# Performance work log

Hardware: AMD Instinct MI355X
Metric: run time of the kernel (lower is better)

Reference implementation:

```python
import jax, jax.numpy as jnp
import numpy as np

N_NODES = 100000

def gcn_conv(x, W, b, src, dst, n_nodes):
    # PyG GCNConv: out = D^{-1/2} (A + I) D^{-1/2} (x W) + b, deg includes self-loop
    h = x @ W  # [N, H]
    ones = jnp.ones(src.shape[0], dtype=x.dtype)
    deg = jax.ops.segment_sum(ones, dst, num_segments=n_nodes) + 1.0  # +1 self-loop
    dinv = jax.lax.rsqrt(deg)  # deg >= 1, no zeros
    norm = dinv[src] * dinv[dst]  # [E]
    msg = h[src] * norm[:, None]  # [E, H] gather + scale
    agg = jax.ops.segment_sum(msg, dst, num_segments=n_nodes)  # scatter-add
    self_contrib = h * (dinv * dinv)[:, None]  # self-loop term norm = dinv_i^2
    return agg + self_contrib + b


def setup_inputs() -> dict:
    key = jax.random.key(0)
    ks = jax.random.split(key, 6)
    F_IN, H, E = 128, 128, 1600000
    x = jax.random.normal(ks[0], (N_NODES, F_IN), dtype=jnp.float32)
    edge_index = jax.random.randint(ks[1], (2, E), 0, N_NODES, dtype=jnp.int32)
    s = 1.0 / np.sqrt(F_IN)
    W1 = jax.random.normal(ks[2], (F_IN, H), dtype=jnp.float32) * s
    b1 = jnp.zeros((H,), dtype=jnp.float32)
    W2 = jax.random.normal(ks[3], (H, H), dtype=jnp.float32) * (1.0 / np.sqrt(H))
    b2 = jnp.zeros((H,), dtype=jnp.float32)
    Wlin = jax.random.normal(ks[4], (H, 1), dtype=jnp.float32) * (1.0 / np.sqrt(H))
    blin = jnp.zeros((1,), dtype=jnp.float32)
    return {"x": x, "edge_index": edge_index, "W1": W1, "b1": b1,
            "W2": W2, "b2": b2, "Wlin": Wlin, "blin": blin}


def reference(x, edge_index, W1, b1, W2, b2, Wlin, blin):
    src, dst = edge_index[0], edge_index[1]
    h = gcn_conv(x, W1, b1, src, dst, N_NODES)
    h = jax.nn.relu(h)
    h = gcn_conv(h, W2, b2, src, dst, N_NODES)
    h = jax.nn.relu(h)
    out = h @ Wlin + blin  # [N, 1]
    return out.squeeze(-1)  # [N]
```

## Files before the change

### kernel.cpp

```cpp
#include <hip/hip_runtime.h>
#include <hip/hip_fp16.h>

#define NFEAT 128

typedef _Float16 v8hf __attribute__((ext_vector_type(8)));
typedef _Float16 v4hf __attribute__((ext_vector_type(4)));
typedef float v4f __attribute__((ext_vector_type(4)));

__global__ void k_deg_rank_w(const int* __restrict__ dst, int* __restrict__ deg,
                             int* __restrict__ rank, int E, int N,
                             const float* __restrict__ W1, const float* __restrict__ W2,
                             _Float16* __restrict__ Wt1, _Float16* __restrict__ Wt2) {
  int e = blockIdx.x * blockDim.x + threadIdx.x;
  if (e < E) rank[e] = atomicAdd(&deg[dst[e]], 1);
  else if (e < E + N) rank[e] = atomicAdd(&deg[e - E], 1);
  else if (e < E + N + 32768) {
    int idx = e - E - N;
    const float* W = (idx < 16384) ? W1 : W2;
    _Float16* Wt = (idx < 16384) ? Wt1 : Wt2;
    int i = idx & 16383;
    int k = i >> 7, n = i & 127;
    Wt[n * 128 + k] = (_Float16)W[k * 128 + n];
  }
}

__device__ __forceinline__ int wave_incl_scan(int v, int lane) {
  #pragma unroll
  for (int off = 1; off < 64; off <<= 1) {
    int t = __shfl_up(v, off, 64);
    if (lane >= off) v += t;
  }
  return v;
}

__global__ __launch_bounds__(256) void k_scan_blocks(const int* __restrict__ deg,
    int* __restrict__ base, int* __restrict__ partials, int n) {
  __shared__ int lds[4];
  const int tid = threadIdx.x;
  const int lane = tid & 63;
  const int wv = tid >> 6;
  int i0 = (blockIdx.x << 9) + (tid << 1);
  int a = (i0 < n) ? deg[i0] : 0;
  int b = (i0 + 1 < n) ? deg[i0 + 1] : 0;
  int inc = wave_incl_scan(a + b, lane);
  if (lane == 63) lds[wv] = inc;
  __syncthreads();
  int woff = 0, tot = 0;
  #pragma unroll
  for (int w = 0; w < 4; w++) {
    int t = lds[w];
    tot += t;
    if (w < wv) woff += t;
  }
  int ex = woff + inc - (a + b);
  const int N1 = n + 1;
  if (i0 < N1) base[i0] = ex;
  if (i0 + 1 < N1) base[i0 + 1] = ex + a;
  if (tid == 255) partials[blockIdx.x] = tot;
}

__global__ __launch_bounds__(256) void k_scan_partials(int* __restrict__ partials,
                                                       int nb) {
  __shared__ int lds[4];
  const int tid = threadIdx.x;
  const int lane = tid & 63;
  const int wv = tid >> 6;
  int v = (tid < nb) ? partials[tid] : 0;
  int inc = wave_incl_scan(v, lane);
  if (lane == 63) lds[wv] = inc;
  __syncthreads();
  int woff = 0;
  #pragma unroll
  for (int w = 0; w < 4; w++) if (w < wv) woff += lds[w];
  if (tid < nb) partials[tid] = woff + inc - v;
}

__global__ void k_finalize_base(int* __restrict__ base, const int* __restrict__ partials,
    const int* __restrict__ deg, float* __restrict__ dinv, int n) {
  int i = blockIdx.x * blockDim.x + threadIdx.x;
  if (i <= n) {
    base[i] += partials[i >> 9];
    if (i < n) dinv[i] = rsqrtf((float)deg[i]);
  }
}

__global__ void k_scatter(const int* __restrict__ src, const int* __restrict__ dst,
    const int* __restrict__ rank, const int* __restrict__ base,
    int* __restrict__ ssrc, int E, int N) {
  int e = blockIdx.x * blockDim.x + threadIdx.x;
  if (e < E) ssrc[base[dst[e]] + rank[e]] = src[e];
  else if (e < E + N) { int n = e - E; ssrc[base[n] + rank[e]] = n; }
}

template <typename AT>
__global__ __launch_bounds__(256) void k_gemm_mfma(
    const AT* __restrict__ A, const _Float16* __restrict__ Wt,
    const float* __restrict__ dinv, _Float16* __restrict__ g16, int N) {
  __shared__ _Float16 As[64][136];
  __shared__ _Float16 Ws[128][136];
  const int tid = threadIdx.x;
  const int row0 = blockIdx.x * 64;

  if (blockIdx.x == 0 && tid < 16) {
    v8hf z;
    #pragma unroll
    for (int j = 0; j < 8; j++) z[j] = (_Float16)0.f;
    *(v8hf*)(g16 + (size_t)N * NFEAT + tid * 8) = z;
  }

  if constexpr (sizeof(AT) == 4) {
    #pragma unroll
    for (int i = 0; i < 8; i++) {
      int idx = tid + i * 256;
      int row = idx >> 5;
      int c4 = idx & 31;
      int gr = row0 + row; gr = (gr < N) ? gr : (N - 1);
      float4 v = *(const float4*)((const float*)A + (size_t)gr * NFEAT + c4 * 4);
      v4hf h;
      h[0] = (_Float16)v.x; h[1] = (_Float16)v.y;
      h[2] = (_Float16)v.z; h[3] = (_Float16)v.w;
      *(v4hf*)&As[row][c4 * 4] = h;
    }
  } else {
    #pragma unroll
    for (int i = 0; i < 4; i++) {
      int idx = tid + i * 256;
      int row = idx >> 4;
      int c8 = idx & 15;
      int gr = row0 + row; gr = (gr < N) ? gr : (N - 1);
      *(uint4*)&As[row][c8 * 8] =
          *(const uint4*)((const _Float16*)A + (size_t)gr * NFEAT + c8 * 8);
    }
  }
  #pragma unroll
  for (int i = 0; i < 8; i++) {
    int idx = tid + i * 256;
    int row = idx >> 4;
    int c8 = idx & 15;
    *(uint4*)&Ws[row][c8 * 8] = *(const uint4*)(Wt + (size_t)row * 128 + c8 * 8);
  }
  __syncthreads();

  const int wv = tid >> 6;
  const int lane = tid & 63;
  const int m = lane & 15;
  const int q = lane >> 4;

  v4f acc[8] = {};
  const _Float16* arow = &As[wv * 16 + m][0];
  #pragma unroll
  for (int kt = 0; kt < 4; kt++) {
    v8hf af = *(const v8hf*)(arow + kt * 32 + q * 8);
    #pragma unroll
    for (int ct = 0; ct < 8; ct++) {
      v8hf bf = *(const v8hf*)(&Ws[ct * 16 + m][kt * 32 + q * 8]);
      acc[ct] = __builtin_amdgcn_mfma_f32_16x16x32_f16(af, bf, acc[ct], 0, 0, 0);
    }
  }

  float dv[4];
  #pragma unroll
  for (int r = 0; r < 4; r++) {
    int nd = row0 + wv * 16 + q * 4 + r;
    int c = (nd < N) ? nd : (N - 1);
    dv[r] = dinv[c];
  }

  __syncthreads();
  #pragma unroll
  for (int ct = 0; ct < 8; ct++)
    #pragma unroll
    for (int r = 0; r < 4; r++)
      As[wv * 16 + q * 4 + r][ct * 16 + m] = (_Float16)(acc[ct][r] * dv[r]);
  __syncthreads();

  #pragma unroll
  for (int i = 0; i < 4; i++) {
    int idx = tid + i * 256;
    int row = idx >> 4;
    int c8 = idx & 15;
    int gr = row0 + row;
    if (gr < N)
      *(v8hf*)(g16 + (size_t)gr * NFEAT + c8 * 8) = *(const v8hf*)&As[row][c8 * 8];
  }
}

__global__ __launch_bounds__(256) void k_agg(
    const _Float16* __restrict__ g, const float* __restrict__ dinv,
    const int* __restrict__ base, const int* __restrict__ ssrc,
    const float* __restrict__ bias, _Float16* __restrict__ hB, int N) {
  const int lane = threadIdx.x & 63;
  const int n = blockIdx.x * 4 + (threadIdx.x >> 6);
  if (n >= N) return;
  const int gq = lane >> 4;
  const int l = lane & 15;
  const int b0 = base[n], b1 = base[n + 1];

  int e = b0;
  int p0 = e + gq, p1 = e + 4 + gq;
  int i0 = ssrc[p0], i1 = ssrc[p1];
  i0 = (p0 < b1) ? i0 : N;
  i1 = (p1 < b1) ? i1 : N;
  v8hf r0 = *(const v8hf*)(g + (size_t)i0 * NFEAT + l * 8);
  v8hf r1 = *(const v8hf*)(g + (size_t)i1 * NFEAT + l * 8);
  int e2 = e + 8;
  int j0 = N, j1 = N;
  if (e2 < b1) {
    int q0 = e2 + gq, q1 = e2 + 4 + gq;
    j0 = ssrc[q0]; j1 = ssrc[q1];
    j0 = (q0 < b1) ? j0 : N;
    j1 = (q1 < b1) ? j1 : N;
  }

  float acc[8] = {};
  while (true) {
    bool more = (e2 < b1);
    v8hf s0, s1;
    if (more) {
      s0 = *(const v8hf*)(g + (size_t)j0 * NFEAT + l * 8);
      s1 = *(const v8hf*)(g + (size_t)j1 * NFEAT + l * 8);
    }
    int e3 = e2 + 8;
    int c0 = N, c1 = N;
    if (e3 < b1) {
      int q0 = e3 + gq, q1 = e3 + 4 + gq;
      c0 = ssrc[q0]; c1 = ssrc[q1];
      c0 = (q0 < b1) ? c0 : N;
      c1 = (q1 < b1) ? c1 : N;
    }
    #pragma unroll
    for (int j = 0; j < 8; j++) acc[j] += (float)r0[j] + (float)r1[j];
    if (!more) break;
    r0 = s0; r1 = s1;
    j0 = c0; j1 = c1;
    e2 = e3;
  }

  #pragma unroll
  for (int j = 0; j < 8; j++) {
    acc[j] += __shfl_xor(acc[j], 16, 64);
    acc[j] += __shfl_xor(acc[j], 32, 64);
  }
  if (gq == 0) {
    float dvn = dinv[n];
    const float* bp = bias + l * 8;
    float4 bb0 = *(const float4*)(bp);
    float4 bb1 = *(const float4*)(bp + 4);
    float bv[8] = {bb0.x, bb0.y, bb0.z, bb0.w, bb1.x, bb1.y, bb1.z, bb1.w};
    v8hf o;
    #pragma unroll
    for (int j = 0; j < 8; j++)
      o[j] = (_Float16)fmaxf(acc[j] * dvn + bv[j], 0.f);
    *(v8hf*)(hB + (size_t)n * NFEAT + l * 8) = o;
  }
}

__global__ __launch_bounds__(256) void k_agg_final(
    const _Float16* __restrict__ g, const float* __restrict__ dinv,
    const int* __restrict__ base, const int* __restrict__ ssrc,
    const float* __restrict__ bias, const float* __restrict__ wlin,
    const float* __restrict__ blin, float* __restrict__ out, int N) {
  const int lane = threadIdx.x & 63;
  const int n = blockIdx.x * 4 + (threadIdx.x >> 6);
  if (n >= N) return;
  const int gq = lane >> 4;
  const int l = lane & 15;
  const int b0 = base[n], b1 = base[n + 1];

  int e = b0;
  int p0 = e + gq, p1 = e + 4 + gq;
  int i0 = ssrc[p0], i1 = ssrc[p1];
  i0 = (p0 < b1) ? i0 : N;
  i1 = (p1 < b1) ? i1 : N;
  v8hf r0 = *(const v8hf*)(g + (size_t)i0 * NFEAT + l * 8);
  v8hf r1 = *(const v8hf*)(g + (size_t)i1 * NFEAT + l * 8);
  int e2 = e + 8;
  int j0 = N, j1 = N;
  if (e2 < b1) {
    int q0 = e2 + gq, q1 = e2 + 4 + gq;
    j0 = ssrc[q0]; j1 = ssrc[q1];
    j0 = (q0 < b1) ? j0 : N;
    j1 = (q1 < b1) ? j1 : N;
  }

  float acc[8] = {};
  while (true) {
    bool more = (e2 < b1);
    v8hf s0, s1;
    if (more) {
      s0 = *(const v8hf*)(g + (size_t)j0 * NFEAT + l * 8);
      s1 = *(const v8hf*)(g + (size_t)j1 * NFEAT + l * 8);
    }
    int e3 = e2 + 8;
    int c0 = N, c1 = N;
    if (e3 < b1) {
      int q0 = e3 + gq, q1 = e3 + 4 + gq;
      c0 = ssrc[q0]; c1 = ssrc[q1];
      c0 = (q0 < b1) ? c0 : N;
      c1 = (q1 < b1) ? c1 : N;
    }
    #pragma unroll
    for (int j = 0; j < 8; j++) acc[j] += (float)r0[j] + (float)r1[j];
    if (!more) break;
    r0 = s0; r1 = s1;
    j0 = c0; j1 = c1;
    e2 = e3;
  }

  #pragma unroll
  for (int j = 0; j < 8; j++) {
    acc[j] += __shfl_xor(acc[j], 16, 64);
    acc[j] += __shfl_xor(acc[j], 32, 64);
  }
  float dvn = dinv[n];
  const float* bp = bias + l * 8;
  const float* wp = wlin + l * 8;
  float4 bb0 = *(const float4*)(bp);
  float4 bb1 = *(const float4*)(bp + 4);
  float4 wl0 = *(const float4*)(wp);
  float4 wl1 = *(const float4*)(wp + 4);
  float bv[8] = {bb0.x, bb0.y, bb0.z, bb0.w, bb1.x, bb1.y, bb1.z, bb1.w};
  float wv[8] = {wl0.x, wl0.y, wl0.z, wl0.w, wl1.x, wl1.y, wl1.z, wl1.w};
  float pv = 0.f;
  #pragma unroll
  for (int j = 0; j < 8; j++)
    pv += fmaxf(acc[j] * dvn + bv[j], 0.f) * wv[j];
  pv += __shfl_xor(pv, 1, 64);
  pv += __shfl_xor(pv, 2, 64);
  pv += __shfl_xor(pv, 4, 64);
  pv += __shfl_xor(pv, 8, 64);
  if (lane == 0) out[n] = pv + blin[0];
}

extern "C" void kernel_launch(void* const* d_in, const int* in_sizes, int n_in,
                              void* d_out, int out_size, void* d_ws, size_t ws_size,
                              hipStream_t stream) {
  const float* x    = (const float*)d_in[0];
  const int*   ei   = (const int*)d_in[1];
  const float* W1   = (const float*)d_in[2];
  const float* b1   = (const float*)d_in[3];
  const float* W2   = (const float*)d_in[4];
  const float* b2   = (const float*)d_in[5];
  const float* Wlin = (const float*)d_in[6];
  const float* blin = (const float*)d_in[7];
  const int N = in_sizes[0] / NFEAT;
  const int E = in_sizes[1] / 2;
  const int* src = ei;
  const int* dst = ei + E;
  const int Etot = E + N;

  int* ws_i = (int*)d_ws;
  size_t off = 0;
  int* deg      = ws_i + off; off += N;
  int* base     = ws_i + off; off += (size_t)N + 1;
  off = (off + 3) & ~(size_t)3;
  int* partials = ws_i + off; off += 256;
  int* ssrc     = ws_i + off; off += Etot + 8;
  float* dinv   = (float*)(ws_i + off); off += N;
  off = (off + 3) & ~(size_t)3;
  _Float16* Wt1 = (_Float16*)(ws_i + off); off += 8192;
  _Float16* Wt2 = (_Float16*)(ws_i + off); off += 8192;
  _Float16* g16 = (_Float16*)(ws_i + off); off += (size_t)(N + 1) * 64;
  _Float16* hB  = (_Float16*)(ws_i + off); off += (size_t)N * 64;
  int* rank     = (int*)g16;

  hipMemsetAsync(deg, 0, (size_t)N * sizeof(int), stream);

  const int tpbE = 256;
  const int gE = (Etot + 32768 + tpbE - 1) / tpbE;
  k_deg_rank_w<<<gE, tpbE, 0, stream>>>(dst, deg, rank, E, N, W1, W2, Wt1, Wt2);

  const int nb = (N + 1 + 511) / 512;
  k_scan_blocks<<<nb, 256, 0, stream>>>(deg, base, partials, N);
  k_scan_partials<<<1, 256, 0, stream>>>(partials, nb);
  k_finalize_base<<<((N + 1) + 255) / 256, 256, 0, stream>>>(base, partials, deg, dinv, N);
  k_scatter<<<(Etot + tpbE - 1) / tpbE, tpbE, 0, stream>>>(src, dst, rank, base, ssrc, E, N);

  const int gg = (N + 63) / 64;
  const int ga = (N + 3) / 4;
  k_gemm_mfma<float><<<gg, 256, 0, stream>>>(x, Wt1, dinv, g16, N);
  k_agg<<<ga, 256, 0, stream>>>(g16, dinv, base, ssrc, b1, hB, N);
  k_gemm_mfma<_Float16><<<gg, 256, 0, stream>>>(hB, Wt2, dinv, g16, N);
  k_agg_final<<<ga, 256, 0, stream>>>(g16, dinv, base, ssrc, b2,
                                      Wlin, blin, (float*)d_out, N);
}
```

Baseline: 373.6 us.

## Fuse scatter with first GEMM and fold scan finalize into consumers

Removes the finalize-base kernel: dinv is now computed in the block-scan kernel, and consumers add the block partial offset to base on the fly. The CSR scatter and the first MFMA GEMM are merged into one launch whose blocks are interleaved, so the memory-bound scatter and the compute-bound GEMM can overlap. The rank buffer moves to hB so it no longer aliases g16, which the fused GEMM writes. This cuts two launches and their serialization, at the cost of an extra partials load per node in the aggregation kernels and higher LDS use for the scatter blocks.

```diff
diff --git a/kernel.cpp b/kernel.cpp
--- a/kernel.cpp
+++ b/kernel.cpp
@@ -34,7 +34,8 @@
 }
 
 __global__ __launch_bounds__(256) void k_scan_blocks(const int* __restrict__ deg,
-    int* __restrict__ base, int* __restrict__ partials, int n) {
+    int* __restrict__ base, int* __restrict__ partials,
+    float* __restrict__ dinv, int n) {
   __shared__ int lds[4];
   const int tid = threadIdx.x;
   const int lane = tid & 63;
@@ -42,6 +43,8 @@
   int i0 = (blockIdx.x << 9) + (tid << 1);
   int a = (i0 < n) ? deg[i0] : 0;
   int b = (i0 + 1 < n) ? deg[i0 + 1] : 0;
+  if (i0 < n) dinv[i0] = rsqrtf((float)a);
+  if (i0 + 1 < n) dinv[i0 + 1] = rsqrtf((float)b);
   int inc = wave_incl_scan(a + b, lane);
   if (lane == 63) lds[wv] = inc;
   __syncthreads();
@@ -75,38 +78,13 @@
   if (tid < nb) partials[tid] = woff + inc - v;
 }
 
-__global__ void k_finalize_base(int* __restrict__ base, const int* __restrict__ partials,
-    const int* __restrict__ deg, float* __restrict__ dinv, int n) {
-  int i = blockIdx.x * blockDim.x + threadIdx.x;
-  if (i <= n) {
-    base[i] += partials[i >> 9];
-    if (i < n) dinv[i] = rsqrtf((float)deg[i]);
-  }
-}
-
-__global__ void k_scatter(const int* __restrict__ src, const int* __restrict__ dst,
-    const int* __restrict__ rank, const int* __restrict__ base,
-    int* __restrict__ ssrc, int E, int N) {
-  int e = blockIdx.x * blockDim.x + threadIdx.x;
-  if (e < E) ssrc[base[dst[e]] + rank[e]] = src[e];
-  else if (e < E + N) { int n = e - E; ssrc[base[n] + rank[e]] = n; }
-}
-
 template <typename AT>
-__global__ __launch_bounds__(256) void k_gemm_mfma(
+__device__ __forceinline__ void gemm_tile(
     const AT* __restrict__ A, const _Float16* __restrict__ Wt,
-    const float* __restrict__ dinv, _Float16* __restrict__ g16, int N) {
-  __shared__ _Float16 As[64][136];
-  __shared__ _Float16 Ws[128][136];
+    const float* __restrict__ dinv, _Float16* __restrict__ g16, int N, int tile,
+    _Float16 (*As)[136], _Float16 (*Ws)[136]) {
   const int tid = threadIdx.x;
-  const int row0 = blockIdx.x * 64;
-
-  if (blockIdx.x == 0 && tid < 16) {
-    v8hf z;
-    #pragma unroll
-    for (int j = 0; j < 8; j++) z[j] = (_Float16)0.f;
-    *(v8hf*)(g16 + (size_t)N * NFEAT + tid * 8) = z;
-  }
+  const int row0 = tile * 64;
 
   if constexpr (sizeof(AT) == 4) {
     #pragma unroll
@@ -185,16 +163,58 @@
   }
 }
 
+__global__ __launch_bounds__(256) void k_sg1(
+    const int* __restrict__ src, const int* __restrict__ dst,
+    const int* __restrict__ rank, const int* __restrict__ base,
+    const int* __restrict__ partials, int* __restrict__ ssrc,
+    const float* __restrict__ x, const _Float16* __restrict__ Wt1,
+    const float* __restrict__ dinv, _Float16* __restrict__ g16,
+    int E, int N, int gg) {
+  __shared__ _Float16 As[64][136];
+  __shared__ _Float16 Ws[128][136];
+  int id = blockIdx.x;
+  if (id < 2 * gg && (id & 1)) {
+    int tile = id >> 1;
+    if (tile == 0 && threadIdx.x < 16) {
+      v8hf z;
+      #pragma unroll
+      for (int j = 0; j < 8; j++) z[j] = (_Float16)0.f;
+      *(v8hf*)(g16 + (size_t)N * NFEAT + threadIdx.x * 8) = z;
+    }
+    gemm_tile<float>(x, Wt1, dinv, g16, N, tile, As, Ws);
+    return;
+  }
+  id = (id < 2 * gg) ? (id >> 1) : (id - gg);
+  int e = id * 256 + threadIdx.x;
+  if (e < E) {
+    int d = dst[e];
+    ssrc[base[d] + partials[d >> 9] + rank[e]] = src[e];
+  } else if (e < E + N) {
+    int nn = e - E;
+    ssrc[base[nn] + partials[nn >> 9] + rank[e]] = nn;
+  }
+}
+
+__global__ __launch_bounds__(256) void k_gemm2(
+    const _Float16* __restrict__ A, const _Float16* __restrict__ Wt,
+    const float* __restrict__ dinv, _Float16* __restrict__ g16, int N) {
+  __shared__ _Float16 As[64][136];
+  __shared__ _Float16 Ws[128][136];
+  gemm_tile<_Float16>(A, Wt, dinv, g16, N, blockIdx.x, As, Ws);
+}
+
 __global__ __launch_bounds__(256) void k_agg(
     const _Float16* __restrict__ g, const float* __restrict__ dinv,
-    const int* __restrict__ base, const int* __restrict__ ssrc,
+    const int* __restrict__ base, const int* __restrict__ partials,
+    const int* __restrict__ ssrc,
     const float* __restrict__ bias, _Float16* __restrict__ hB, int N) {
   const int lane = threadIdx.x & 63;
   const int n = blockIdx.x * 4 + (threadIdx.x >> 6);
   if (n >= N) return;
   const int gq = lane >> 4;
   const int l = lane & 15;
-  const int b0 = base[n], b1 = base[n + 1];
+  const int b0 = base[n] + partials[n >> 9];
+  const int b1 = base[n + 1] + partials[(n + 1) >> 9];
 
   int e = b0;
   int p0 = e + gq, p1 = e + 4 + gq;
@@ -257,7 +277,8 @@
 
 __global__ __launch_bounds__(256) void k_agg_final(
     const _Float16* __restrict__ g, const float* __restrict__ dinv,
-    const int* __restrict__ base, const int* __restrict__ ssrc,
+    const int* __restrict__ base, const int* __restrict__ partials,
+    const int* __restrict__ ssrc,
     const float* __restrict__ bias, const float* __restrict__ wlin,
     const float* __restrict__ blin, float* __restrict__ out, int N) {
   const int lane = threadIdx.x & 63;
@@ -265,7 +286,8 @@
   if (n >= N) return;
   const int gq = lane >> 4;
   const int l = lane & 15;
-  const int b0 = base[n], b1 = base[n + 1];
+  const int b0 = base[n] + partials[n >> 9];
+  const int b1 = base[n + 1] + partials[(n + 1) >> 9];
 
   int e = b0;
   int p0 = e + gq, p1 = e + 4 + gq;
@@ -362,7 +384,7 @@
   _Float16* Wt2 = (_Float16*)(ws_i + off); off += 8192;
   _Float16* g16 = (_Float16*)(ws_i + off); off += (size_t)(N + 1) * 64;
   _Float16* hB  = (_Float16*)(ws_i + off); off += (size_t)N * 64;
-  int* rank     = (int*)g16;
+  int* rank = (int*)hB;
 
   hipMemsetAsync(deg, 0, (size_t)N * sizeof(int), stream);
 
@@ -371,16 +393,16 @@
   k_deg_rank_w<<<gE, tpbE, 0, stream>>>(dst, deg, rank, E, N, W1, W2, Wt1, Wt2);
 
   const int nb = (N + 1 + 511) / 512;
-  k_scan_blocks<<<nb, 256, 0, stream>>>(deg, base, partials, N);
+  k_scan_blocks<<<nb, 256, 0, stream>>>(deg, base, partials, dinv, N);
   k_scan_partials<<<1, 256, 0, stream>>>(partials, nb);
-  k_finalize_base<<<((N + 1) + 255) / 256, 256, 0, stream>>>(base, partials, deg, dinv, N);
-  k_scatter<<<(Etot + tpbE - 1) / tpbE, tpbE, 0, stream>>>(src, dst, rank, base, ssrc, E, N);
 
   const int gg = (N + 63) / 64;
   const int ga = (N + 3) / 4;
-  k_gemm_mfma<float><<<gg, 256, 0, stream>>>(x, Wt1, dinv, g16, N);
-  k_agg<<<ga, 256, 0, stream>>>(g16, dinv, base, ssrc, b1, hB, N);
-  k_gemm_mfma<_Float16><<<gg, 256, 0, stream>>>(hB, Wt2, dinv, g16, N);
-  k_agg_final<<<ga, 256, 0, stream>>>(g16, dinv, base, ssrc, b2,
+  const int scb = (Etot + 255) / 256;
+  k_sg1<<<scb + gg, 256, 0, stream>>>(src, dst, rank, base, partials, ssrc,
+                                      x, Wt1, dinv, g16, E, N, gg);
+  k_agg<<<ga, 256, 0, stream>>>(g16, dinv, base, partials, ssrc, b1, hB, N);
+  k_gemm2<<<gg, 256, 0, stream>>>(hB, Wt2, dinv, g16, N);
+  k_agg_final<<<ga, 256, 0, stream>>>(g16, dinv, base, partials, ssrc, b2,
                                       Wlin, blin, (float*)d_out, N);
 }
```

After: 376.3 us. No clear change (+0.7%).

## Replace global-atomic CSR build with two-level bucketed counting sort

Applied to the files above, without the earlier changes.

Building the CSR no longer relies on per-edge global atomics on a degree array plus a multi-kernel scan. Edges are first bucketed by destination into 512-node buckets, using a block-local LDS histogram, a single-block scan and a scatter of packed (dst,src) pairs. A per-bucket kernel then counts degrees, scans, computes dinv and places sources with LDS atomics. This cuts contended global atomics and random global writes, but adds an 8-byte-per-edge intermediate pass and limits the node count to 256 buckets.

```diff
diff --git a/kernel.cpp b/kernel.cpp
--- a/kernel.cpp
+++ b/kernel.cpp
@@ -2,94 +2,173 @@
 #include <hip/hip_fp16.h>
 
 #define NFEAT 128
+#define BSH 9
+#define BSZ 512
+#define EPB 2048
 
 typedef _Float16 v8hf __attribute__((ext_vector_type(8)));
 typedef _Float16 v4hf __attribute__((ext_vector_type(4)));
 typedef float v4f __attribute__((ext_vector_type(4)));
 
-__global__ void k_deg_rank_w(const int* __restrict__ dst, int* __restrict__ deg,
-                             int* __restrict__ rank, int E, int N,
-                             const float* __restrict__ W1, const float* __restrict__ W2,
-                             _Float16* __restrict__ Wt1, _Float16* __restrict__ Wt2) {
-  int e = blockIdx.x * blockDim.x + threadIdx.x;
-  if (e < E) rank[e] = atomicAdd(&deg[dst[e]], 1);
-  else if (e < E + N) rank[e] = atomicAdd(&deg[e - E], 1);
-  else if (e < E + N + 32768) {
-    int idx = e - E - N;
+__device__ __forceinline__ int wave_incl_scan(int v, int lane) {
+  #pragma unroll
+  for (int off = 1; off < 64; off <<= 1) {
+    int t = __shfl_up(v, off, 64);
+    if (lane >= off) v += t;
+  }
+  return v;
+}
+
+__global__ __launch_bounds__(256) void k_wt(
+    const float* __restrict__ W1, const float* __restrict__ W2,
+    _Float16* __restrict__ Wt1, _Float16* __restrict__ Wt2,
+    int* __restrict__ ghist) {
+  int idx = blockIdx.x * 256 + threadIdx.x;
+  if (idx < 32768) {
     const float* W = (idx < 16384) ? W1 : W2;
     _Float16* Wt = (idx < 16384) ? Wt1 : Wt2;
     int i = idx & 16383;
     int k = i >> 7, n = i & 127;
     Wt[n * 128 + k] = (_Float16)W[k * 128 + n];
-  }
-}
-
-__device__ __forceinline__ int wave_incl_scan(int v, int lane) {
-  #pragma unroll
-  for (int off = 1; off < 64; off <<= 1) {
-    int t = __shfl_up(v, off, 64);
-    if (lane >= off) v += t;
-  }
-  return v;
-}
-
-__global__ __launch_bounds__(256) void k_scan_blocks(const int* __restrict__ deg,
-    int* __restrict__ base, int* __restrict__ partials, int n) {
-  __shared__ int lds[4];
+  } else if (idx < 32768 + 256) {
+    ghist[idx - 32768] = 0;
+  }
+}
+
+__global__ __launch_bounds__(256) void k_bhist(const int* __restrict__ dst,
+                                               int* __restrict__ ghist, int E) {
+  __shared__ int h[256];
+  const int tid = threadIdx.x;
+  h[tid] = 0;
+  __syncthreads();
+  int e0 = blockIdx.x * EPB;
+  #pragma unroll
+  for (int i = 0; i < EPB / 256; i++) {
+    int e = e0 + tid + i * 256;
+    if (e < E) atomicAdd(&h[dst[e] >> BSH], 1);
+  }
+  __syncthreads();
+  int c = h[tid];
+  if (c) atomicAdd(&ghist[tid], c);
+}
+
+__global__ __launch_bounds__(256) void k_bscan(
+    const int* __restrict__ ghist, int* __restrict__ ebase,
+    int* __restrict__ sbase, int* __restrict__ cursor,
+    int* __restrict__ base, int nb, int N) {
+  __shared__ int l1[4], l2[4];
   const int tid = threadIdx.x;
   const int lane = tid & 63;
   const int wv = tid >> 6;
-  int i0 = (blockIdx.x << 9) + (tid << 1);
-  int a = (i0 < n) ? deg[i0] : 0;
-  int b = (i0 + 1 < n) ? deg[i0 + 1] : 0;
-  int inc = wave_incl_scan(a + b, lane);
-  if (lane == 63) lds[wv] = inc;
-  __syncthreads();
-  int woff = 0, tot = 0;
-  #pragma unroll
-  for (int w = 0; w < 4; w++) {
-    int t = lds[w];
-    tot += t;
-    if (w < wv) woff += t;
-  }
-  int ex = woff + inc - (a + b);
-  const int N1 = n + 1;
-  if (i0 < N1) base[i0] = ex;
-  if (i0 + 1 < N1) base[i0 + 1] = ex + a;
-  if (tid == 255) partials[blockIdx.x] = tot;
-}
-
-__global__ __launch_bounds__(256) void k_scan_partials(int* __restrict__ partials,
-                                                       int nb) {
+  int ve = (tid < nb) ? ghist[tid] : 0;
+  int selfc = 0;
+  if (tid < nb) {
+    int rem = N - (tid << BSH);
+    selfc = (rem < BSZ) ? rem : BSZ;
+  }
+  int vs = ve + selfc;
+  int ie = wave_incl_scan(ve, lane);
+  int is = wave_incl_scan(vs, lane);
+  if (lane == 63) { l1[wv] = ie; l2[wv] = is; }
+  __syncthreads();
+  int we = 0, ws = 0;
+  #pragma unroll
+  for (int w = 0; w < 4; w++) if (w < wv) { we += l1[w]; ws += l2[w]; }
+  if (tid <= nb) {
+    int eb = we + ie - ve;
+    ebase[tid] = eb;
+    cursor[tid] = eb;
+    sbase[tid] = ws + is - vs;
+    if (tid == nb) base[N] = ws + is - vs;
+  }
+}
+
+__global__ __launch_bounds__(256) void k_bscatter(
+    const int* __restrict__ src, const int* __restrict__ dst,
+    int* __restrict__ cursor, unsigned long long* __restrict__ epk, int E) {
+  __shared__ int h[256];
+  __shared__ int res[256];
+  const int tid = threadIdx.x;
+  h[tid] = 0;
+  __syncthreads();
+  int e0 = blockIdx.x * EPB;
+  #pragma unroll
+  for (int i = 0; i < EPB / 256; i++) {
+    int e = e0 + tid + i * 256;
+    if (e < E) atomicAdd(&h[dst[e] >> BSH], 1);
+  }
+  __syncthreads();
+  int c = h[tid];
+  if (c) res[tid] = atomicAdd(&cursor[tid], c);
+  __syncthreads();
+  h[tid] = 0;
+  __syncthreads();
+  #pragma unroll
+  for (int i = 0; i < EPB / 256; i++) {
+    int e = e0 + tid + i * 256;
+    if (e < E) {
+      int d = dst[e];
+      int b = d >> BSH;
+      int off = atomicAdd(&h[b], 1);
+      epk[res[b] + off] =
+          ((unsigned long long)(unsigned)d << 32) | (unsigned)src[e];
+    }
+  }
+}
+
+__global__ __launch_bounds__(256) void k_bfinal(
+    const unsigned long long* __restrict__ epk, const int* __restrict__ ebase,
+    const int* __restrict__ sbase, int* __restrict__ base,
+    float* __restrict__ dinv, int* __restrict__ ssrc, int N) {
+  __shared__ int cnt[BSZ];
+  __shared__ int ex[BSZ];
   __shared__ int lds[4];
+  const int k = blockIdx.x;
   const int tid = threadIdx.x;
   const int lane = tid & 63;
   const int wv = tid >> 6;
-  int v = (tid < nb) ? partials[tid] : 0;
-  int inc = wave_incl_scan(v, lane);
+  const int n0 = k << BSH;
+
+  #pragma unroll
+  for (int i = tid; i < BSZ; i += 256) cnt[i] = (n0 + i < N) ? 1 : 0;
+  __syncthreads();
+  const int eb = ebase[k], ee = ebase[k + 1];
+  for (int e = eb + tid; e < ee; e += 256) {
+    int d = (int)(epk[e] >> 32);
+    atomicAdd(&cnt[d - n0], 1);
+  }
+  __syncthreads();
+  int a = cnt[2 * tid], b = cnt[2 * tid + 1];
+  int inc = wave_incl_scan(a + b, lane);
   if (lane == 63) lds[wv] = inc;
   __syncthreads();
   int woff = 0;
   #pragma unroll
   for (int w = 0; w < 4; w++) if (w < wv) woff += lds[w];
-  if (tid < nb) partials[tid] = woff + inc - v;
-}
-
-__global__ void k_finalize_base(int* __restrict__ base, const int* __restrict__ partials,
-    const int* __restrict__ deg, float* __restrict__ dinv, int n) {
-  int i = blockIdx.x * blockDim.x + threadIdx.x;
-  if (i <= n) {
-    base[i] += partials[i >> 9];
-    if (i < n) dinv[i] = rsqrtf((float)deg[i]);
-  }
-}
-
-__global__ void k_scatter(const int* __restrict__ src, const int* __restrict__ dst,
-    const int* __restrict__ rank, const int* __restrict__ base,
-    int* __restrict__ ssrc, int E, int N) {
-  int e = blockIdx.x * blockDim.x + threadIdx.x;
-  if (e < E) ssrc[base[dst[e]] + rank[e]] = src[e];
-  else if (e < E + N) { int n = e - E; ssrc[base[n] + rank[e]] = n; }
+  int e0x = woff + inc - (a + b);
+  ex[2 * tid] = e0x;
+  ex[2 * tid + 1] = e0x + a;
+  __syncthreads();
+
+  const int sb = sbase[k];
+  #pragma unroll
+  for (int i = tid; i < BSZ; i += 256) {
+    int n = n0 + i;
+    if (n <= N) base[n] = sb + ex[i];
+    if (n < N) {
+      dinv[n] = rsqrtf((float)cnt[i]);
+      ssrc[sb + ex[i]] = n;
+      ex[i] = ex[i] + 1;
+    }
+  }
+  __syncthreads();
+  for (int e = eb + tid; e < ee; e += 256) {
+    unsigned long long p = epk[e];
+    int d = (int)(p >> 32);
+    int s = (int)(p & 0xffffffffu);
+    int off = atomicAdd(&ex[d - n0], 1);
+    ssrc[sb + off] = s;
+  }
 }
 
 template <typename AT>
@@ -348,33 +427,31 @@
   const int* src = ei;
   const int* dst = ei + E;
   const int Etot = E + N;
+  const int nb = (N + BSZ - 1) >> BSH;
 
   int* ws_i = (int*)d_ws;
   size_t off = 0;
-  int* deg      = ws_i + off; off += N;
-  int* base     = ws_i + off; off += (size_t)N + 1;
-  off = (off + 3) & ~(size_t)3;
-  int* partials = ws_i + off; off += 256;
-  int* ssrc     = ws_i + off; off += Etot + 8;
-  float* dinv   = (float*)(ws_i + off); off += N;
+  int* base    = ws_i + off; off += (size_t)N + 1;
+  int* ghist   = ws_i + off; off += 256;
+  int* ebase   = ws_i + off; off += 257;
+  int* sbase   = ws_i + off; off += 257;
+  int* cursor  = ws_i + off; off += 257;
+  int* ssrc    = ws_i + off; off += Etot + 16;
+  float* dinv  = (float*)(ws_i + off); off += N;
   off = (off + 3) & ~(size_t)3;
   _Float16* Wt1 = (_Float16*)(ws_i + off); off += 8192;
   _Float16* Wt2 = (_Float16*)(ws_i + off); off += 8192;
   _Float16* g16 = (_Float16*)(ws_i + off); off += (size_t)(N + 1) * 64;
+  off = (off + 1) & ~(size_t)1;
   _Float16* hB  = (_Float16*)(ws_i + off); off += (size_t)N * 64;
-  int* rank     = (int*)g16;
-
-  hipMemsetAsync(deg, 0, (size_t)N * sizeof(int), stream);
-
-  const int tpbE = 256;
-  const int gE = (Etot + 32768 + tpbE - 1) / tpbE;
-  k_deg_rank_w<<<gE, tpbE, 0, stream>>>(dst, deg, rank, E, N, W1, W2, Wt1, Wt2);
-
-  const int nb = (N + 1 + 511) / 512;
-  k_scan_blocks<<<nb, 256, 0, stream>>>(deg, base, partials, N);
-  k_scan_partials<<<1, 256, 0, stream>>>(partials, nb);
-  k_finalize_base<<<((N + 1) + 255) / 256, 256, 0, stream>>>(base, partials, deg, dinv, N);
-  k_scatter<<<(Etot + tpbE - 1) / tpbE, tpbE, 0, stream>>>(src, dst, rank, base, ssrc, E, N);
+  unsigned long long* epk = (unsigned long long*)hB;
+
+  k_wt<<<129, 256, 0, stream>>>(W1, W2, Wt1, Wt2, ghist);
+  const int ebg = (E + EPB - 1) / EPB;
+  k_bhist<<<ebg, 256, 0, stream>>>(dst, ghist, E);
+  k_bscan<<<1, 256, 0, stream>>>(ghist, ebase, sbase, cursor, base, nb, N);
+  k_bscatter<<<ebg, 256, 0, stream>>>(src, dst, cursor, epk, E);
+  k_bfinal<<<nb, 256, 0, stream>>>(epk, ebase, sbase, base, dinv, ssrc, N);
 
   const int gg = (N + 63) / 64;
   const int ga = (N + 3) / 4;
```

New measurement: 359.8 us, median of 2. 1.04x faster.
